# Kernel optimization log

Hardware: AMD Instinct MI355X
Metric: run time of the kernel (lower is better)

The kernel has to match this reference:

```python
import jax, jax.numpy as jnp
import numpy as np
from jax import lax


def setup_inputs() -> dict:
    key = jax.random.key(0)
    k1, k2, k3, k4, k5 = jax.random.split(key, 5)
    B, T, V, E, U = 64, 256, 32000, 256, 1024
    x = jax.random.randint(k1, (B, T), 0, V)          # token ids; 0 = pad (mask_zero=True)
    hidden = jnp.zeros((B, U), dtype=jnp.float32)      # initialize_hidden_state()
    emb = jax.random.normal(k2, (V, E), dtype=jnp.float32) * 0.05
    W = jax.random.normal(k3, (E, 3 * U), dtype=jnp.float32) * 0.05   # input kernel [z|r|h]
    Uk = jax.random.normal(k4, (U, 3 * U), dtype=jnp.float32) * 0.05  # recurrent kernel
    b = jax.random.normal(k5, (2, 3 * U), dtype=jnp.float32) * 0.05   # [input_bias, recurrent_bias] (reset_after=True)
    return {"x": x, "hidden": hidden, "emb": emb, "W": W, "U": Uk, "b": b}


def reference(x, hidden, emb, W, U, b):
    # Embedding with mask_zero=True: mask out pad tokens in the GRU scan.
    mask = (x != 0)                              # [B, T] bool
    xe = emb[x]                                  # [B, T, E]
    # Precompute all input projections in one big GEMM.
    xproj = jnp.einsum("bte,eu->btu", xe, W) + b[0]   # [B, T, 3U]
    nU = U.shape[0]

    def step(h, inp):
        xp, m = inp                              # xp: [B, 3U], m: [B]
        rec = h @ U + b[1]                       # [B, 3U]
        xz, xr, xh = jnp.split(xp, 3, axis=-1)
        rz, rr, rh = jnp.split(rec, 3, axis=-1)
        z = jax.nn.sigmoid(xz + rz)
        r = jax.nn.sigmoid(xr + rr)
        hh = jnp.tanh(xh + r * rh)               # reset_after=True form
        h_new = z * h + (1.0 - z) * hh
        h_new = jnp.where(m[:, None], h_new, h)  # masked steps carry state/output through
        return h_new, h_new

    state, outs = lax.scan(step, hidden,
                           (jnp.swapaxes(xproj, 0, 1), jnp.swapaxes(mask, 0, 1)))
    output = jnp.swapaxes(outs, 0, 1)            # [B, T, U]
    return output, state
```

## Files before the change

kernel.cpp:

```cpp
#include <hip/hip_runtime.h>
#include <hip/hip_cooperative_groups.h>

#define BB 64
#define TT 256
#define EE 256
#define NU 1024
#define N3 3072

typedef __attribute__((ext_vector_type(8))) short bf16x8;
typedef __attribute__((ext_vector_type(4))) float f32x4;

__device__ __forceinline__ unsigned short f2bf(float f) {
    unsigned u = __float_as_uint(f);
    return (unsigned short)((u + 0x7FFFu + ((u >> 16) & 1u)) >> 16);
}

__global__ __launch_bounds__(256) void upack_kernel(
    const float* __restrict__ U, float* __restrict__ up)
{
    __shared__ float t32[32][33];
    const int c0 = blockIdx.x * 32, k0 = blockIdx.y * 32;
    const int tx = threadIdx.x & 31, ty = threadIdx.x >> 5;
    #pragma unroll
    for (int i = 0; i < 4; ++i) {
        int k = ty + i * 8;
        t32[k][tx] = U[(size_t)(k0 + k) * N3 + c0 + tx];
    }
    __syncthreads();
    #pragma unroll
    for (int i = 0; i < 4; ++i) {
        int cl = ty + i * 8;
        int c = c0 + cl;
        int u = c & 1023, g = c >> 10;
        up[(size_t)(u * 3 + g) * NU + k0 + tx] = t32[tx][cl];
    }
}

__global__ __launch_bounds__(64) void tokT_kernel(
    const int* __restrict__ x, int* __restrict__ xT)
{
    const int t = blockIdx.x, b = threadIdx.x;
    xT[t * BB + b] = x[b * TT + t];
}

__global__ __launch_bounds__(256) void hinit_kernel(
    const float* __restrict__ hidden, unsigned short* __restrict__ hb0,
    unsigned* __restrict__ cnt)
{
    const int u = blockIdx.x * 4 + (threadIdx.x >> 6);
    const int b = threadIdx.x & 63;
    hb0[((u >> 3) * 64 + b) * 8 + (u & 7)] = f2bf(hidden[(size_t)b * NU + u]);
    if (blockIdx.x == 0) {
        cnt[threadIdx.x] = 0u;
        cnt[threadIdx.x + 256] = 0u;
    }
}

__global__ __launch_bounds__(256) void xprojT_kernel(
    const int* __restrict__ x, const float* __restrict__ emb,
    const float* __restrict__ W, const float* __restrict__ bias,
    float* __restrict__ xpT)
{
    __shared__ float AsT[32][132];
    __shared__ float Ws[32][132];
    __shared__ int toks[128];

    const int tid = threadIdx.x;
    const int mt = blockIdx.x / 24, nt = blockIdx.x % 24;
    const int m0 = mt * 128, n0 = nt * 128;

    if (tid < 128) {
        int mg = m0 + tid;
        toks[tid] = x[(mg & 63) * TT + (mg >> 6)];
    }
    __syncthreads();

    const int tx = tid & 15, ty = tid >> 4;
    float acc[8][8] = {};

    for (int kb = 0; kb < 8; ++kb) {
        const int k0 = kb * 32;
        if (kb) __syncthreads();
        #pragma unroll
        for (int i = 0; i < 4; ++i) {
            int idx = tid + 256 * i;
            int m = idx >> 3, c4 = idx & 7;
            float4 av = *(const float4*)(emb + (size_t)toks[m] * EE + k0 + c4 * 4);
            AsT[c4 * 4 + 0][m] = av.x; AsT[c4 * 4 + 1][m] = av.y;
            AsT[c4 * 4 + 2][m] = av.z; AsT[c4 * 4 + 3][m] = av.w;
            int r = idx >> 5, w4 = idx & 31;
            *(float4*)&Ws[r][w4 * 4] =
                *(const float4*)(W + (size_t)(k0 + r) * N3 + n0 + w4 * 4);
        }
        __syncthreads();
        #pragma unroll 8
        for (int kk = 0; kk < 32; ++kk) {
            float a8[8], w8[8];
            *(float4*)a8       = *(const float4*)&AsT[kk][ty * 8];
            *(float4*)(a8 + 4) = *(const float4*)&AsT[kk][ty * 8 + 4];
            *(float4*)w8       = *(const float4*)&Ws[kk][tx * 8];
            *(float4*)(w8 + 4) = *(const float4*)&Ws[kk][tx * 8 + 4];
            #pragma unroll
            for (int i = 0; i < 8; ++i)
                #pragma unroll
                for (int j = 0; j < 8; ++j) acc[i][j] += a8[i] * w8[j];
        }
    }

    float b8[8];
    *(float4*)b8       = *(const float4*)(bias + n0 + tx * 8);
    *(float4*)(b8 + 4) = *(const float4*)(bias + n0 + tx * 8 + 4);
    const int t0 = mt * 2 + (ty >> 3);
    const int bb0 = (ty & 7) * 8;
    #pragma unroll
    for (int j = 0; j < 8; ++j) {
        const int c = n0 + tx * 8 + j;
        float4 lo, hi;
        lo.x = acc[0][j] + b8[j]; lo.y = acc[1][j] + b8[j];
        lo.z = acc[2][j] + b8[j]; lo.w = acc[3][j] + b8[j];
        hi.x = acc[4][j] + b8[j]; hi.y = acc[5][j] + b8[j];
        hi.z = acc[6][j] + b8[j]; hi.w = acc[7][j] + b8[j];
        size_t base = ((size_t)t0 * N3 + c) * BB + bb0;
        *(float4*)(xpT + base)     = lo;
        *(float4*)(xpT + base + 4) = hi;
    }
}

__global__ __launch_bounds__(512) void gru_persist(
    const int* __restrict__ xT, const float* __restrict__ upack,
    const float* __restrict__ bias, float* xpT,
    float* __restrict__ out, const float* __restrict__ hidden,
    unsigned short* hb0, unsigned short* hb1, unsigned* cnt)
{
    __shared__ f32x4 red2[6144];
    __shared__ unsigned short hstage[64 * 20];

    const int tid = threadIdx.x;
    const int U0 = blockIdx.x * 16;
    const int w = tid >> 6;
    const int lane = tid & 63;

    const int gdu = tid >> 5;
    const int gbA = tid & 31;

    bf16x8 af[3][4];
    {
        const int du = lane & 15;
        #pragma unroll
        for (int g = 0; g < 3; ++g)
            #pragma unroll
            for (int s = 0; s < 4; ++s) {
                const int k0 = w * 128 + s * 32 + (lane >> 4) * 8;
                const float* p = upack + (size_t)((U0 + du) * 3 + g) * NU + k0;
                float4 v0 = *(const float4*)p;
                float4 v1 = *(const float4*)(p + 4);
                af[g][s] = (bf16x8){ (short)f2bf(v0.x), (short)f2bf(v0.y),
                                     (short)f2bf(v0.z), (short)f2bf(v0.w),
                                     (short)f2bf(v1.x), (short)f2bf(v1.y),
                                     (short)f2bf(v1.z), (short)f2bf(v1.w) };
            }
    }

    float holdA = hidden[(size_t)gbA * NU + U0 + gdu];
    float holdB = hidden[(size_t)(gbA + 32) * NU + U0 + gdu];
    const float brz = bias[N3 + 0 * NU + U0 + gdu];
    const float brr = bias[N3 + 1 * NU + U0 + gdu];
    const float brh = bias[N3 + 2 * NU + U0 + gdu];
    float xzA, xrA, xhA, xzB, xrB, xhB; int tokA, tokB;
    {
        size_t xb = ((size_t)0 * N3 + U0 + gdu) * BB + gbA;
        xzA = xpT[xb];                      xzB = xpT[xb + 32];
        xrA = xpT[xb + (size_t)NU * BB];    xrB = xpT[xb + (size_t)NU * BB + 32];
        xhA = xpT[xb + (size_t)2 * NU * BB];xhB = xpT[xb + (size_t)2 * NU * BB + 32];
        tokA = xT[0 * BB + gbA];            tokB = xT[0 * BB + gbA + 32];
    }
    float* state_out = out + (size_t)BB * TT * NU;
    __syncthreads();

    const unsigned short* hc = hb0;
    unsigned short* hn = hb1;

    for (int t = 0; t < TT; ++t) {
        bf16x8 bv[4][4];
        #pragma unroll
        for (int n = 0; n < 4; ++n)
            #pragma unroll
            for (int s = 0; s < 4; ++s) {
                const int ew = w * 16 + s * 4 + (lane >> 4);
                bv[n][s] = *(const bf16x8*)(hc +
                    (size_t)(ew * 64 + n * 16 + (lane & 15)) * 8);
            }

        f32x4 c[3][4];
        #pragma unroll
        for (int g = 0; g < 3; ++g)
            #pragma unroll
            for (int n = 0; n < 4; ++n) c[g][n] = (f32x4){0.f, 0.f, 0.f, 0.f};
        #pragma unroll
        for (int s = 0; s < 4; ++s)
            #pragma unroll
            for (int g = 0; g < 3; ++g)
                #pragma unroll
                for (int n = 0; n < 4; ++n)
                    c[g][n] = __builtin_amdgcn_mfma_f32_16x16x32_bf16(
                        af[g][s], bv[n][s], c[g][n], 0, 0, 0);

        #pragma unroll
        for (int g = 0; g < 3; ++g)
            #pragma unroll
            for (int n = 0; n < 4; ++n)
                red2[((w * 3 + g) * 4 + n) * 64 + lane] = c[g][n];
        __syncthreads();

        {
            const int lA = (gdu >> 2) * 16 + (gbA & 15);
            const int rsub = gdu & 3;
            const int nA = gbA >> 4;
            float rzA = brz, rrA = brr, rhA = brh;
            float rzB = brz, rrB = brr, rhB = brh;
            #pragma unroll
            for (int q = 0; q < 8; ++q) {
                const int qb = (q * 3) * 4;
                float vA, vB;
                vA = ((const float*)&red2[(qb + 0 * 4 + nA) * 64 + lA])[rsub];
                vB = ((const float*)&red2[(qb + 0 * 4 + nA + 2) * 64 + lA])[rsub];
                rzA += vA; rzB += vB;
                vA = ((const float*)&red2[(qb + 1 * 4 + nA) * 64 + lA])[rsub];
                vB = ((const float*)&red2[(qb + 1 * 4 + nA + 2) * 64 + lA])[rsub];
                rrA += vA; rrB += vB;
                vA = ((const float*)&red2[(qb + 2 * 4 + nA) * 64 + lA])[rsub];
                vB = ((const float*)&red2[(qb + 2 * 4 + nA + 2) * 64 + lA])[rsub];
                rhA += vA; rhB += vB;
            }
            float zA  = 1.f / (1.f + expf(-(xzA + rzA)));
            float rA  = 1.f / (1.f + expf(-(xrA + rrA)));
            float hhA = tanhf(xhA + rA * rhA);
            float hnewA = zA * holdA + (1.f - zA) * hhA;
            if (tokA == 0) hnewA = holdA;
            float zB  = 1.f / (1.f + expf(-(xzB + rzB)));
            float rB  = 1.f / (1.f + expf(-(xrB + rrB)));
            float hhB = tanhf(xhB + rB * rhB);
            float hnewB = zB * holdB + (1.f - zB) * hhB;
            if (tokB == 0) hnewB = holdB;

            size_t ob = ((size_t)t * N3 + U0 + gdu) * BB + gbA;
            __hip_atomic_store(&xpT[ob], hnewA,
                               __ATOMIC_RELAXED, __HIP_MEMORY_SCOPE_SYSTEM);
            __hip_atomic_store(&xpT[ob + 32], hnewB,
                               __ATOMIC_RELAXED, __HIP_MEMORY_SCOPE_SYSTEM);
            if (t == TT - 1) {
                __hip_atomic_store(&state_out[(size_t)gbA * NU + U0 + gdu], hnewA,
                                   __ATOMIC_RELAXED, __HIP_MEMORY_SCOPE_SYSTEM);
                __hip_atomic_store(&state_out[(size_t)(gbA + 32) * NU + U0 + gdu], hnewB,
                                   __ATOMIC_RELAXED, __HIP_MEMORY_SCOPE_SYSTEM);
            }
            hstage[gbA * 20 + gdu] = f2bf(hnewA);
            hstage[(gbA + 32) * 20 + gdu] = f2bf(hnewB);
            holdA = hnewA; holdB = hnewB;
        }
        __syncthreads();

        if (w == 4 || w == 5) {
            const int g2 = w - 4;
            unsigned long long lo =
                *(const unsigned long long*)&hstage[lane * 20 + 8 * g2];
            unsigned long long hi =
                *(const unsigned long long*)&hstage[lane * 20 + 8 * g2 + 4];
            unsigned short* dst = hn + ((size_t)((U0 >> 3) + g2) * 64 + lane) * 8;
            __hip_atomic_store((unsigned long long*)dst, lo,
                               __ATOMIC_RELAXED, __HIP_MEMORY_SCOPE_SYSTEM);
            __hip_atomic_store((unsigned long long*)(dst + 4), hi,
                               __ATOMIC_RELAXED, __HIP_MEMORY_SCOPE_SYSTEM);
        }

        __builtin_amdgcn_s_waitcnt(0);
        __syncthreads();

        if (t + 1 < TT) {
            size_t xb = ((size_t)(t + 1) * N3 + U0 + gdu) * BB + gbA;
            xzA = xpT[xb];                      xzB = xpT[xb + 32];
            xrA = xpT[xb + (size_t)NU * BB];    xrB = xpT[xb + (size_t)NU * BB + 32];
            xhA = xpT[xb + (size_t)2 * NU * BB];xhB = xpT[xb + (size_t)2 * NU * BB + 32];
            tokA = xT[(t + 1) * BB + gbA];      tokB = xT[(t + 1) * BB + gbA + 32];
        }

        if (tid == 0) {
            const unsigned g = (unsigned)blockIdx.x >> 3;
            __hip_atomic_fetch_add(&cnt[g * 32], 1u,
                                   __ATOMIC_RELAXED, __HIP_MEMORY_SCOPE_SYSTEM);
            const unsigned tgt = 8u * ((unsigned)t + 1u);
            unsigned mn;
            long guard = 0;
            do {
                mn = 0xffffffffu;
                #pragma unroll
                for (int g8 = 0; g8 < 8; ++g8) {
                    unsigned v = __hip_atomic_load(&cnt[g8 * 32],
                                  __ATOMIC_RELAXED, __HIP_MEMORY_SCOPE_SYSTEM);
                    mn = v < mn ? v : mn;
                }
                if (mn < tgt) __builtin_amdgcn_s_sleep(1);
            } while (mn < tgt && ++guard < (1L << 24));
            __builtin_amdgcn_fence(__ATOMIC_ACQUIRE, "");
        }
        __syncthreads();

        const unsigned short* tmp = hc; hc = hn; hn = (unsigned short*)tmp;
    }
}

__global__ __launch_bounds__(256) void outT_kernel(
    const float* __restrict__ xpT, float* __restrict__ out)
{
    __shared__ float tile[64][65];
    const int t = blockIdx.x, u0 = blockIdx.y * 64;
    const int lane = threadIdx.x & 63, row = threadIdx.x >> 6;
    #pragma unroll
    for (int r = row; r < 64; r += 4)
        tile[r][lane] = xpT[((size_t)t * N3 + u0 + r) * BB + lane];
    __syncthreads();
    #pragma unroll
    for (int b = row; b < 64; b += 4)
        out[((size_t)b * TT + t) * NU + u0 + lane] = tile[lane][b];
}

extern "C" void kernel_launch(void* const* d_in, const int* in_sizes, int n_in,
                              void* d_out, int out_size, void* d_ws, size_t ws_size,
                              hipStream_t stream) {
    const int*   x      = (const int*)d_in[0];
    const float* hidden = (const float*)d_in[1];
    const float* emb    = (const float*)d_in[2];
    const float* W      = (const float*)d_in[3];
    const float* U      = (const float*)d_in[4];
    const float* bvec   = (const float*)d_in[5];

    float* out = (float*)d_out;

    float*          xpT   = (float*)d_ws;
    float*          upck  = xpT + (size_t)16384 * N3;
    unsigned short* hb0   = (unsigned short*)(upck + (size_t)3 * NU * NU);
    unsigned short* hb1   = hb0 + (size_t)NU * BB;
    int*            xT    = (int*)(hb1 + (size_t)NU * BB);
    unsigned*       cnt   = (unsigned*)(xT + TT * BB);

    upack_kernel<<<dim3(96, 32), dim3(256), 0, stream>>>(U, upck);
    tokT_kernel<<<dim3(TT), dim3(64), 0, stream>>>(x, xT);
    hinit_kernel<<<dim3(256), dim3(256), 0, stream>>>(hidden, hb0, cnt);
    xprojT_kernel<<<dim3(3072), dim3(256), 0, stream>>>(x, emb, W, bvec, xpT);

    void* args[] = {(void*)&xT, (void*)&upck, (void*)&bvec, (void*)&xpT,
                    (void*)&out, (void*)&hidden, (void*)&hb0, (void*)&hb1,
                    (void*)&cnt};
    hipLaunchCooperativeKernel((const void*)gru_persist, dim3(64), dim3(512),
                               args, 0, stream);

    outT_kernel<<<dim3(TT, 16), dim3(256), 0, stream>>>(xpT, out);
}
```

Measured before the change: 2.051 ms.

## Parallelize cross-wave reduction, defer output stores, drop acquire fence

The cross-wave reduction of the recurrent GEMM partials becomes a parallel tree step: every thread sums eight wave partials into a small shared buffer, and the gate phase then reads one value per gate instead of looping over eight. The output store of each step's hidden state is moved to the start of the next step, and the final state is written after the loop, taking stores off the critical path before the barrier. The acquire fence after the grid-wide spin-wait is removed and the hidden-state loads become relaxed system-scope atomics. This relies on relaxed atomics alone to give correct cross-block visibility, and it adds one extra __syncthreads per step.

```diff
diff --git a/kernel.cpp b/kernel.cpp
--- a/kernel.cpp
+++ b/kernel.cpp
@@ -133,6 +133,7 @@
     unsigned short* hb0, unsigned short* hb1, unsigned* cnt)
 {
     __shared__ f32x4 red2[6144];
+    __shared__ f32x4 redS[768];
     __shared__ unsigned short hstage[64 * 20];
 
     const int tid = threadIdx.x;
@@ -181,14 +182,28 @@
     unsigned short* hn = hb1;
 
     for (int t = 0; t < TT; ++t) {
+        if (t > 0) {
+            size_t ob = ((size_t)(t - 1) * N3 + U0 + gdu) * BB + gbA;
+            __hip_atomic_store(&xpT[ob], holdA,
+                               __ATOMIC_RELAXED, __HIP_MEMORY_SCOPE_SYSTEM);
+            __hip_atomic_store(&xpT[ob + 32], holdB,
+                               __ATOMIC_RELAXED, __HIP_MEMORY_SCOPE_SYSTEM);
+        }
+
         bf16x8 bv[4][4];
         #pragma unroll
         for (int n = 0; n < 4; ++n)
             #pragma unroll
             for (int s = 0; s < 4; ++s) {
                 const int ew = w * 16 + s * 4 + (lane >> 4);
-                bv[n][s] = *(const bf16x8*)(hc +
+                const unsigned long long* hq = (const unsigned long long*)(hc +
                     (size_t)(ew * 64 + n * 16 + (lane & 15)) * 8);
+                union { unsigned long long q[2]; bf16x8 v; } uu;
+                uu.q[0] = __hip_atomic_load(hq, __ATOMIC_RELAXED,
+                                            __HIP_MEMORY_SCOPE_SYSTEM);
+                uu.q[1] = __hip_atomic_load(hq + 1, __ATOMIC_RELAXED,
+                                            __HIP_MEMORY_SCOPE_SYSTEM);
+                bv[n][s] = uu.v;
             }
 
         f32x4 c[3][4];
@@ -209,29 +224,35 @@
         for (int g = 0; g < 3; ++g)
             #pragma unroll
             for (int n = 0; n < 4; ++n)
-                red2[((w * 3 + g) * 4 + n) * 64 + lane] = c[g][n];
+                red2[(w * 12 + g * 4 + n) * 64 + lane] = c[g][n];
+        __syncthreads();
+
+        {
+            f32x4 s0 = red2[tid];
+            #pragma unroll
+            for (int q = 1; q < 8; ++q) s0 += red2[q * 768 + tid];
+            redS[tid] = s0;
+            if (tid < 256) {
+                const int o2 = 512 + tid;
+                f32x4 s1 = red2[o2];
+                #pragma unroll
+                for (int q = 1; q < 8; ++q) s1 += red2[q * 768 + o2];
+                redS[o2] = s1;
+            }
+        }
         __syncthreads();
 
         {
             const int lA = (gdu >> 2) * 16 + (gbA & 15);
             const int rsub = gdu & 3;
             const int nA = gbA >> 4;
-            float rzA = brz, rrA = brr, rhA = brh;
-            float rzB = brz, rrB = brr, rhB = brh;
-            #pragma unroll
-            for (int q = 0; q < 8; ++q) {
-                const int qb = (q * 3) * 4;
-                float vA, vB;
-                vA = ((const float*)&red2[(qb + 0 * 4 + nA) * 64 + lA])[rsub];
-                vB = ((const float*)&red2[(qb + 0 * 4 + nA + 2) * 64 + lA])[rsub];
-                rzA += vA; rzB += vB;
-                vA = ((const float*)&red2[(qb + 1 * 4 + nA) * 64 + lA])[rsub];
-                vB = ((const float*)&red2[(qb + 1 * 4 + nA + 2) * 64 + lA])[rsub];
-                rrA += vA; rrB += vB;
-                vA = ((const float*)&red2[(qb + 2 * 4 + nA) * 64 + lA])[rsub];
-                vB = ((const float*)&red2[(qb + 2 * 4 + nA + 2) * 64 + lA])[rsub];
-                rhA += vA; rhB += vB;
-            }
+            float rzA = brz + ((const float*)&redS[(0 * 4 + nA) * 64 + lA])[rsub];
+            float rrA = brr + ((const float*)&redS[(1 * 4 + nA) * 64 + lA])[rsub];
+            float rhA = brh + ((const float*)&redS[(2 * 4 + nA) * 64 + lA])[rsub];
+            float rzB = brz + ((const float*)&redS[(0 * 4 + nA + 2) * 64 + lA])[rsub];
+            float rrB = brr + ((const float*)&redS[(1 * 4 + nA + 2) * 64 + lA])[rsub];
+            float rhB = brh + ((const float*)&redS[(2 * 4 + nA + 2) * 64 + lA])[rsub];
+
             float zA  = 1.f / (1.f + expf(-(xzA + rzA)));
             float rA  = 1.f / (1.f + expf(-(xrA + rrA)));
             float hhA = tanhf(xhA + rA * rhA);
@@ -243,17 +264,6 @@
             float hnewB = zB * holdB + (1.f - zB) * hhB;
             if (tokB == 0) hnewB = holdB;
 
-            size_t ob = ((size_t)t * N3 + U0 + gdu) * BB + gbA;
-            __hip_atomic_store(&xpT[ob], hnewA,
-                               __ATOMIC_RELAXED, __HIP_MEMORY_SCOPE_SYSTEM);
-            __hip_atomic_store(&xpT[ob + 32], hnewB,
-                               __ATOMIC_RELAXED, __HIP_MEMORY_SCOPE_SYSTEM);
-            if (t == TT - 1) {
-                __hip_atomic_store(&state_out[(size_t)gbA * NU + U0 + gdu], hnewA,
-                                   __ATOMIC_RELAXED, __HIP_MEMORY_SCOPE_SYSTEM);
-                __hip_atomic_store(&state_out[(size_t)(gbA + 32) * NU + U0 + gdu], hnewB,
-                                   __ATOMIC_RELAXED, __HIP_MEMORY_SCOPE_SYSTEM);
-            }
             hstage[gbA * 20 + gdu] = f2bf(hnewA);
             hstage[(gbA + 32) * 20 + gdu] = f2bf(hnewB);
             holdA = hnewA; holdB = hnewB;
@@ -301,11 +311,22 @@
                 }
                 if (mn < tgt) __builtin_amdgcn_s_sleep(1);
             } while (mn < tgt && ++guard < (1L << 24));
-            __builtin_amdgcn_fence(__ATOMIC_ACQUIRE, "");
         }
         __syncthreads();
 
         const unsigned short* tmp = hc; hc = hn; hn = (unsigned short*)tmp;
+    }
+
+    {
+        size_t ob = ((size_t)(TT - 1) * N3 + U0 + gdu) * BB + gbA;
+        __hip_atomic_store(&xpT[ob], holdA,
+                           __ATOMIC_RELAXED, __HIP_MEMORY_SCOPE_SYSTEM);
+        __hip_atomic_store(&xpT[ob + 32], holdB,
+                           __ATOMIC_RELAXED, __HIP_MEMORY_SCOPE_SYSTEM);
+        __hip_atomic_store(&state_out[(size_t)gbA * NU + U0 + gdu], holdA,
+                           __ATOMIC_RELAXED, __HIP_MEMORY_SCOPE_SYSTEM);
+        __hip_atomic_store(&state_out[(size_t)(gbA + 32) * NU + U0 + gdu], holdB,
+                           __ATOMIC_RELAXED, __HIP_MEMORY_SCOPE_SYSTEM);
     }
 }
 
```

Measured after the change: 2.135 ms. 1.04x slower.
